# Performance work log

Hardware: AMD Instinct MI355X
Metric: run time of the kernel (lower is better)

The kernel has to match this reference:

```python
import jax, jax.numpy as jnp
import numpy as np

EMB_DIM = 1024
N_HEAD = 16
HEAD_DIM = EMB_DIM // N_HEAD


def setup_inputs() -> dict:
    key = jax.random.key(0)
    kx, kq, kk, kv, ko = jax.random.split(key, 5)
    B, S = 4, 2048
    x = jax.random.normal(kx, (B, S, EMB_DIM), dtype=jnp.float32)
    attention_mask = jnp.ones((B, S), dtype=jnp.int32)
    s = 1.0 / np.sqrt(EMB_DIM)
    w_q = jax.random.normal(kq, (EMB_DIM, EMB_DIM), dtype=jnp.float32) * s
    w_k = jax.random.normal(kk, (EMB_DIM, EMB_DIM), dtype=jnp.float32) * s
    w_v = jax.random.normal(kv, (EMB_DIM, EMB_DIM), dtype=jnp.float32) * s
    w_o = jax.random.normal(ko, (EMB_DIM, EMB_DIM), dtype=jnp.float32) * s
    return {"x": x, "attention_mask": attention_mask,
            "w_q": w_q, "w_k": w_k, "w_v": w_v, "w_o": w_o}


def reference(x, attention_mask, w_q, w_k, w_v, w_o):
    B, S, _ = x.shape
    scale = 1.0 / np.sqrt(HEAD_DIM)
    # projections; nn.Linear computes x @ W^T
    def split_heads(t):
        return t.reshape(B, S, N_HEAD, HEAD_DIM).transpose(0, 2, 1, 3)  # [B,H,S,D]
    q = split_heads(x @ w_q.T)
    k = split_heads(x @ w_k.T)
    v = split_heads(x @ w_v.T)
    scores = jnp.einsum('bhqd,bhkd->bhqk', q, k) * scale  # [B,H,S,S]
    pad_mask = (attention_mask == 0)[:, None, None, :]          # [B,1,1,S]
    causal = jnp.triu(jnp.ones((S, S), dtype=bool), k=1)[None, None]  # [1,1,S,S]
    combined = pad_mask | causal
    scores = jnp.where(combined, -jnp.inf, scores)
    attn = jax.nn.softmax(scores, axis=-1)
    out = jnp.einsum('bhqk,bhkd->bhqd', attn, v)
    out = out.transpose(0, 2, 1, 3).reshape(B, S, EMB_DIM)
    return out @ w_o.T
```

## Files before the change

### kernel.cpp

```cpp
#include <hip/hip_runtime.h>

typedef __bf16 bf16x8 __attribute__((ext_vector_type(8)));
typedef float f32x4 __attribute__((ext_vector_type(4)));

#define LOG2E 1.4426950408889634f
#define NEGC (-12.0f * LOG2E)

__device__ inline unsigned short f2bf(float f) {
  unsigned int u = __builtin_bit_cast(unsigned int, f);
  u += 0x7fff + ((u >> 16) & 1);
  return (unsigned short)(u >> 16);
}

__device__ inline void async16(const void* g, void* l) {
  __builtin_amdgcn_global_load_lds(
      (__attribute__((address_space(1))) void*)(g),
      (__attribute__((address_space(3))) void*)(l), 16, 0, 0);
}

__global__ __launch_bounds__(256) void cast_f32_bf16(
    const float* __restrict__ in, unsigned short* __restrict__ out) {
  int i = (blockIdx.x * 256 + threadIdx.x) * 4;
  float4 v = *(const float4*)(in + i);
  ushort4 o;
  o.x = f2bf(v.x); o.y = f2bf(v.y); o.z = f2bf(v.z); o.w = f2bf(v.w);
  *(ushort4*)(out + i) = o;
}

__global__ __launch_bounds__(256) void cast_w4(
    const float* __restrict__ w0, const float* __restrict__ w1,
    const float* __restrict__ w2, const float* __restrict__ w3,
    unsigned short* __restrict__ o0, unsigned short* __restrict__ o1,
    unsigned short* __restrict__ o2, unsigned short* __restrict__ o3) {
  const float* in; unsigned short* out;
  switch (blockIdx.y) {
    case 0: in = w0; out = o0; break;
    case 1: in = w1; out = o1; break;
    case 2: in = w2; out = o2; break;
    default: in = w3; out = o3; break;
  }
  int i = (blockIdx.x * 256 + threadIdx.x) * 4;
  float4 v = *(const float4*)(in + i);
  ushort4 o;
  o.x = f2bf(v.x); o.y = f2bf(v.y); o.z = f2bf(v.z); o.w = f2bf(v.w);
  *(ushort4*)(out + i) = o;
}

#define BM 128
#define BN 128
#define BK 32

__global__ __launch_bounds__(256, 2) void gemm_bt(
    const unsigned short* __restrict__ A, const unsigned short* __restrict__ W,
    void* __restrict__ out, int M, int N, int K, int mode) {
  __shared__ unsigned short As[BM * BK];
  __shared__ unsigned short Ws[BN * BK];
  int tid = threadIdx.x;
  int lane = tid & 63, wid = tid >> 6;
  int wm = wid >> 1, wn = wid & 1;
  int l15 = lane & 15, quad = lane >> 4;
  int m0 = blockIdx.y * BM, n0 = blockIdx.x * BN;

  f32x4 acc[4][4] = {};

  int srow = tid >> 2;
  int scol = (tid & 3) * 8;
  const unsigned short* Ag = A + (long)(m0 + srow) * K + scol;
  const unsigned short* Wg = W + (long)(n0 + srow) * K + scol;
  char* AsB = (char*)As + wid * 1024;
  char* WsB = (char*)Ws + wid * 1024;

  for (int kt = 0; kt < K; kt += BK) {
    __syncthreads();
    async16(Ag + kt, AsB);
    async16(Ag + kt + (long)64 * K, AsB + 4096);
    async16(Wg + kt, WsB);
    async16(Wg + kt + (long)64 * K, WsB + 4096);
    __syncthreads();
    bf16x8 af[4], wf[4];
#pragma unroll
    for (int t = 0; t < 4; t++)
      af[t] = *(const bf16x8*)(As + (wm * 64 + t * 16 + l15) * BK + quad * 8);
#pragma unroll
    for (int t = 0; t < 4; t++)
      wf[t] = *(const bf16x8*)(Ws + (wn * 64 + t * 16 + l15) * BK + quad * 8);
#pragma unroll
    for (int i = 0; i < 4; i++)
#pragma unroll
      for (int j = 0; j < 4; j++)
        acc[i][j] = __builtin_amdgcn_mfma_f32_16x16x32_bf16(af[i], wf[j], acc[i][j], 0, 0, 0);
  }

  if (mode == 0) {
    float* Cf = (float*)out;
#pragma unroll
    for (int i = 0; i < 4; i++) {
      int row = m0 + wm * 64 + i * 16 + quad * 4;
#pragma unroll
      for (int j = 0; j < 4; j++) {
        int col = n0 + wn * 64 + j * 16 + l15;
#pragma unroll
        for (int r = 0; r < 4; r++)
          Cf[(long)(row + r) * N + col] = acc[i][j][r];
      }
    }
  } else {
    unsigned short* Cb = (unsigned short*)out;
    int which = n0 >> 10;
    if (which == 2) {
#pragma unroll
      for (int i = 0; i < 4; i++)
#pragma unroll
        for (int j = 0; j < 4; j++) {
          int m = m0 + wm * 64 + i * 16 + quad * 4;
          int n = n0 + wn * 64 + j * 16 + l15;
          int nn = n & 1023;
          int b = m >> 11, s = m & 2047;
          int h = nn >> 6, d = nn & 63;
          ushort4 pk;
          pk.x = f2bf(acc[i][j][0]); pk.y = f2bf(acc[i][j][1]);
          pk.z = f2bf(acc[i][j][2]); pk.w = f2bf(acc[i][j][3]);
          *(ushort4*)(&Cb[16777216 + (((long)((b * 16 + h) * 64 + d)) << 11) + s]) = pk;
        }
    } else {
      float scale = (which == 0) ? 0.125f : 1.0f;
#pragma unroll
      for (int i = 0; i < 4; i++)
#pragma unroll
        for (int j = 0; j < 4; j++)
#pragma unroll
          for (int r = 0; r < 4; r++) {
            int m = m0 + wm * 64 + i * 16 + quad * 4 + r;
            int n = n0 + wn * 64 + j * 16 + l15;
            int b = m >> 11, s = m & 2047;
            int nn = n & 1023;
            int h = nn >> 6, d = nn & 63;
            long idx = (long)which * 8388608 + ((long)((b * 16 + h) * 2048 + s)) * 64 + d;
            Cb[idx] = f2bf(acc[i][j][r] * scale);
          }
    }
  }
}

#define BQ 128
#define BKV 64
#define PSTR 76

__global__ __launch_bounds__(256, 4) void attn(
    const unsigned short* __restrict__ Q, const unsigned short* __restrict__ Kt,
    const unsigned short* __restrict__ VT, const int* __restrict__ am,
    unsigned short* __restrict__ O) {
  __shared__ unsigned short QPs[BQ * PSTR];
  __shared__ unsigned short Ks[BKV * PSTR];
  __shared__ unsigned short Vs[64 * PSTR];
  const int S = 2048, D = 64;
  int tid = threadIdx.x, lane = tid & 63, wid = tid >> 6;
  int l15 = lane & 15, quad = lane >> 4;

  int id = blockIdx.x;
  int s = id >> 8;
  int r = id & 255;
  int bh = r & 63;
  int c = r >> 6;
  int qt;
  switch (s) { case 0: qt = c; break; case 1: qt = 7 - c; break;
               case 2: qt = 8 + c; break; default: qt = 15 - c; }
  int q0 = qt * BQ;
  int b = bh >> 4, h = bh & 15;
  const unsigned short* Qg = Q + (long)bh * S * D;
  const unsigned short* Kg = Kt + (long)bh * S * D;
  const unsigned short* Vg = VT + (long)bh * D * S;
  const int* amg = am + b * S;

  int row0 = tid >> 3, col0 = (tid & 7) * 8;
  int row1 = 32 + (tid >> 3), col1 = col0;

#pragma unroll
  for (int rr = 0; rr < 4; rr++) {
    int cc = rr * 256 + tid;
    int row = cc >> 3, col = (cc & 7) * 8;
    *(uint4*)(&QPs[row * PSTR + col]) = *(const uint4*)(Qg + (long)(q0 + row) * D + col);
  }

  uint4 kreg0 = *(const uint4*)(Kg + (long)row0 * D + col0);
  uint4 kreg1 = *(const uint4*)(Kg + (long)row1 * D + col1);
  uint4 vreg0 = *(const uint4*)(Vg + (long)row0 * S + col0);
  uint4 vreg1 = *(const uint4*)(Vg + (long)row1 * S + col1);

  __syncthreads();
  bf16x8 qf[2][2];
#pragma unroll
  for (int i = 0; i < 2; i++)
#pragma unroll
    for (int kk = 0; kk < 2; kk++)
      qf[i][kk] = *(const bf16x8*)(&QPs[(wid * 32 + i * 16 + l15) * PSTR + kk * 32 + quad * 8]);

  f32x4 o_acc[2][4] = {};
  float lsum[2][4] = {};

  int tFull = q0 >> 6;
  int nt = tFull + 2;
  for (int t = 0; t < nt; t++) {
    int s0 = t * BKV;
    __syncthreads();
    *(uint4*)(&Ks[row0 * PSTR + col0]) = kreg0;
    *(uint4*)(&Ks[row1 * PSTR + col1]) = kreg1;
    *(uint4*)(&Vs[row0 * PSTR + col0]) = vreg0;
    *(uint4*)(&Vs[row1 * PSTR + col1]) = vreg1;
    __syncthreads();

    {
      long s0n = (t + 1) * BKV; if (s0n > S - BKV) s0n = S - BKV;
      kreg0 = *(const uint4*)(Kg + (s0n + row0) * D + col0);
      kreg1 = *(const uint4*)(Kg + (s0n + row1) * D + col1);
      vreg0 = *(const uint4*)(Vg + (long)row0 * S + s0n + col0);
      vreg1 = *(const uint4*)(Vg + (long)row1 * S + s0n + col1);
    }

    int mvj[4];
#pragma unroll
    for (int j = 0; j < 4; j++) mvj[j] = amg[s0 + j * 16 + l15];

    f32x4 sacc[2][4] = {};
#pragma unroll
    for (int kk = 0; kk < 2; kk++) {
      bf16x8 kf[4];
#pragma unroll
      for (int j = 0; j < 4; j++)
        kf[j] = *(const bf16x8*)(&Ks[(j * 16 + l15) * PSTR + kk * 32 + quad * 8]);
#pragma unroll
      for (int i = 0; i < 2; i++)
#pragma unroll
        for (int j = 0; j < 4; j++)
          sacc[i][j] = __builtin_amdgcn_mfma_f32_16x16x32_bf16(qf[i][kk], kf[j], sacc[i][j], 0, 0, 0);
    }

    float fb[4];
#pragma unroll
    for (int j = 0; j < 4; j++) fb[j] = mvj[j] ? NEGC : -1e38f;

    if (t < tFull) {
#pragma unroll
      for (int i = 0; i < 2; i++)
#pragma unroll
        for (int rr = 0; rr < 4; rr++) {
          int prow = (wid * 32 + i * 16 + quad * 4 + rr) * PSTR;
          float rs = 0.f;
#pragma unroll
          for (int j = 0; j < 4; j++) {
            float p = __builtin_amdgcn_exp2f(fmaf(sacc[i][j][rr], LOG2E, fb[j]));
            unsigned int u = __builtin_bit_cast(unsigned int, p);
            QPs[prow + j * 16 + l15] = (unsigned short)(u >> 16);
            rs += __builtin_bit_cast(float, u & 0xffff0000u);
          }
          lsum[i][rr] += rs;
        }
    } else {
#pragma unroll
      for (int i = 0; i < 2; i++)
#pragma unroll
        for (int rr = 0; rr < 4; rr++) {
          int row = q0 + wid * 32 + i * 16 + quad * 4 + rr;
          int prow = (wid * 32 + i * 16 + quad * 4 + rr) * PSTR;
          float rs = 0.f;
#pragma unroll
          for (int j = 0; j < 4; j++) {
            int col = s0 + j * 16 + l15;
            float fbe = (col > row) ? -1e38f : fb[j];
            float p = __builtin_amdgcn_exp2f(fmaf(sacc[i][j][rr], LOG2E, fbe));
            unsigned int u = __builtin_bit_cast(unsigned int, p);
            QPs[prow + j * 16 + l15] = (unsigned short)(u >> 16);
            rs += __builtin_bit_cast(float, u & 0xffff0000u);
          }
          lsum[i][rr] += rs;
        }
    }

#pragma unroll
    for (int kk = 0; kk < 2; kk++) {
      bf16x8 pf[2], vf[4];
#pragma unroll
      for (int i = 0; i < 2; i++)
        pf[i] = *(const bf16x8*)(&QPs[(wid * 32 + i * 16 + l15) * PSTR + kk * 32 + quad * 8]);
#pragma unroll
      for (int j = 0; j < 4; j++)
        vf[j] = *(const bf16x8*)(&Vs[(j * 16 + l15) * PSTR + kk * 32 + quad * 8]);
#pragma unroll
      for (int i = 0; i < 2; i++)
#pragma unroll
        for (int j = 0; j < 4; j++)
          o_acc[i][j] = __builtin_amdgcn_mfma_f32_16x16x32_bf16(pf[i], vf[j], o_acc[i][j], 0, 0, 0);
    }
  }

#pragma unroll
  for (int i = 0; i < 2; i++)
#pragma unroll
    for (int rr = 0; rr < 4; rr++) {
      float tsum = lsum[i][rr];
      tsum += __shfl_xor(tsum, 1, 64);
      tsum += __shfl_xor(tsum, 2, 64);
      tsum += __shfl_xor(tsum, 4, 64);
      tsum += __shfl_xor(tsum, 8, 64);
      float inv = 1.0f / tsum;
      int prow = (wid * 32 + i * 16 + quad * 4 + rr) * PSTR;
#pragma unroll
      for (int j = 0; j < 4; j++)
        QPs[prow + j * 16 + l15] = f2bf(o_acc[i][j][rr] * inv);
    }
  __syncthreads();
#pragma unroll
  for (int rr = 0; rr < 4; rr++) {
    int cc = rr * 256 + tid;
    int row = cc >> 3, col = (cc & 7) * 8;
    uint4 v = *(const uint4*)(&QPs[row * PSTR + col]);
    long gm = (long)b * S + q0 + row;
    *(uint4*)(&O[gm * 1024 + h * 64 + col]) = v;
  }
}

extern "C" void kernel_launch(void* const* d_in, const int* in_sizes, int n_in,
                              void* d_out, int out_size, void* d_ws, size_t ws_size,
                              hipStream_t stream) {
  const float* x  = (const float*)d_in[0];
  const int*   am = (const int*)d_in[1];
  const float* wq = (const float*)d_in[2];
  const float* wk = (const float*)d_in[3];
  const float* wv = (const float*)d_in[4];
  const float* wo = (const float*)d_in[5];
  float* out = (float*)d_out;

  const int S = 2048, E = 1024, Bb = 4, H = 16;
  const int M = Bb * S;

  char* ws = (char*)d_ws;
  unsigned short* xb  = (unsigned short*)ws;
  unsigned short* wqb = (unsigned short*)(ws + 16777216);
  unsigned short* wkb = wqb + 1048576;
  unsigned short* wvb = wkb + 1048576;
  unsigned short* wob = wvb + 1048576;
  unsigned short* Qb  = (unsigned short*)(ws + 25165824);
  unsigned short* Ob  = Qb + 25165824;

  cast_f32_bf16<<<M * E / 1024, 256, 0, stream>>>(x, xb);
  cast_w4<<<dim3(E * E / 1024, 4), 256, 0, stream>>>(wq, wk, wv, wo, wqb, wkb, wvb, wob);

  gemm_bt<<<dim3(3 * E / BN, M / BM), 256, 0, stream>>>(xb, wqb, Qb, M, 3 * E, E, 4);
  attn<<<dim3(1024), 256, 0, stream>>>(Qb, Qb + 8388608, Qb + 16777216, am, Ob);
  gemm_bt<<<dim3(E / BN, M / BM), 256, 0, stream>>>(Ob, wob, out, M, E, E, 0);
}
```

Baseline: 297.6 us.

## Merge cast kernels, raise GEMM occupancy, and remap GEMM blocks M-fastest

Folds the activation cast and the four weight casts into one launch, which removes one kernel launch and its gap. Raises the GEMM launch_bounds minimum from 2 to 3 blocks per CU so more blocks can be resident. Flattens the GEMM grid to 1D and walks M tiles first, so consecutive blocks share the same weight tile, which changes L2 reuse. The higher occupancy target may force register spills in the MFMA accumulator loop.

New measurement: 293.1 us. About the same (-1.5%).

```diff
diff --git a/kernel.cpp b/kernel.cpp
--- a/kernel.cpp
+++ b/kernel.cpp
@@ -18,39 +18,34 @@
       (__attribute__((address_space(3))) void*)(l), 16, 0, 0);
 }
 
-__global__ __launch_bounds__(256) void cast_f32_bf16(
-    const float* __restrict__ in, unsigned short* __restrict__ out) {
-  int i = (blockIdx.x * 256 + threadIdx.x) * 4;
+__global__ __launch_bounds__(256) void cast_all(
+    const float* __restrict__ x, const float* __restrict__ w0,
+    const float* __restrict__ w1, const float* __restrict__ w2,
+    const float* __restrict__ w3, unsigned short* __restrict__ xb,
+    unsigned short* __restrict__ ob ) {
+  int id = blockIdx.x;
+  const float* in;
+  unsigned short* out;
+  int boff;
+  if (id < 8192) { in = x; out = xb; boff = id; }
+  else {
+    int w = (id - 8192) >> 10; boff = (id - 8192) & 1023;
+    switch (w) { case 0: in = w0; break; case 1: in = w1; break;
+                 case 2: in = w2; break; default: in = w3; }
+    out = ob + (long)w * 1048576;
+  }
+  int i = (boff * 256 + threadIdx.x) * 4;
   float4 v = *(const float4*)(in + i);
   ushort4 o;
   o.x = f2bf(v.x); o.y = f2bf(v.y); o.z = f2bf(v.z); o.w = f2bf(v.w);
   *(ushort4*)(out + i) = o;
 }
 
-__global__ __launch_bounds__(256) void cast_w4(
-    const float* __restrict__ w0, const float* __restrict__ w1,
-    const float* __restrict__ w2, const float* __restrict__ w3,
-    unsigned short* __restrict__ o0, unsigned short* __restrict__ o1,
-    unsigned short* __restrict__ o2, unsigned short* __restrict__ o3) {
-  const float* in; unsigned short* out;
-  switch (blockIdx.y) {
-    case 0: in = w0; out = o0; break;
-    case 1: in = w1; out = o1; break;
-    case 2: in = w2; out = o2; break;
-    default: in = w3; out = o3; break;
-  }
-  int i = (blockIdx.x * 256 + threadIdx.x) * 4;
-  float4 v = *(const float4*)(in + i);
-  ushort4 o;
-  o.x = f2bf(v.x); o.y = f2bf(v.y); o.z = f2bf(v.z); o.w = f2bf(v.w);
-  *(ushort4*)(out + i) = o;
-}
-
 #define BM 128
 #define BN 128
 #define BK 32
 
-__global__ __launch_bounds__(256, 2) void gemm_bt(
+__global__ __launch_bounds__(256, 3) void gemm_bt(
     const unsigned short* __restrict__ A, const unsigned short* __restrict__ W,
     void* __restrict__ out, int M, int N, int K, int mode) {
   __shared__ unsigned short As[BM * BK];
@@ -59,7 +54,7 @@
   int lane = tid & 63, wid = tid >> 6;
   int wm = wid >> 1, wn = wid & 1;
   int l15 = lane & 15, quad = lane >> 4;
-  int m0 = blockIdx.y * BM, n0 = blockIdx.x * BN;
+  int m0 = (blockIdx.x & 63) * BM, n0 = (blockIdx.x >> 6) * BN;
 
   f32x4 acc[4][4] = {};
 
@@ -336,16 +331,13 @@
   char* ws = (char*)d_ws;
   unsigned short* xb  = (unsigned short*)ws;
   unsigned short* wqb = (unsigned short*)(ws + 16777216);
-  unsigned short* wkb = wqb + 1048576;
-  unsigned short* wvb = wkb + 1048576;
-  unsigned short* wob = wvb + 1048576;
+  unsigned short* wob = wqb + 3 * 1048576;
   unsigned short* Qb  = (unsigned short*)(ws + 25165824);
   unsigned short* Ob  = Qb + 25165824;
 
-  cast_f32_bf16<<<M * E / 1024, 256, 0, stream>>>(x, xb);
-  cast_w4<<<dim3(E * E / 1024, 4), 256, 0, stream>>>(wq, wk, wv, wo, wqb, wkb, wvb, wob);
-
-  gemm_bt<<<dim3(3 * E / BN, M / BM), 256, 0, stream>>>(xb, wqb, Qb, M, 3 * E, E, 4);
+  cast_all<<<12288, 256, 0, stream>>>(x, wq, wk, wv, wo, xb, wqb);
+
+  gemm_bt<<<dim3((3 * E / BN) * (M / BM)), 256, 0, stream>>>(xb, wqb, Qb, M, 3 * E, E, 4);
   attn<<<dim3(1024), 256, 0, stream>>>(Qb, Qb + 8388608, Qb + 16777216, am, Ob);
-  gemm_bt<<<dim3(E / BN, M / BM), 256, 0, stream>>>(Ob, wob, out, M, E, E, 0);
-}
+  gemm_bt<<<dim3((E / BN) * (M / BM)), 256, 0, stream>>>(Ob, wob, out, M, E, E, 0);
+}
```
